# Kernel optimization log

Measured on AMD Instinct MI355X. Metric: run time of the kernel, lower is better.

Reference implementation:

```python
import jax, jax.numpy as jnp
import numpy as np

# Standard FP4 E2M1 lookup table (nvfp4-style): sign bit in nibble MSB.
FP4_LUT = jnp.array([0.0, 0.5, 1.0, 1.5, 2.0, 3.0, 4.0, 6.0,
                     -0.0, -0.5, -1.0, -1.5, -2.0, -3.0, -4.0, -6.0],
                    dtype=jnp.float32)


def dequant_fp4(packed_i32, scales, group_size):
    """packed_i32: [K/8, N] int32 (8 fp4 nibbles per word, low nibble first);
    scales: [K/group_size, N]. Returns dense fp32 weight [K, N]."""
    w = jax.lax.bitcast_convert_type(packed_i32, jnp.uint32)  # [K/8, N]
    # Unpack nibbles along the reduction axis: nibble i -> row 8*r + i.
    nib = jnp.stack([(w >> jnp.uint32(4 * i)) & jnp.uint32(0xF) for i in range(8)],
                    axis=1)                                    # [K/8, 8, N]
    K = nib.shape[0] * 8
    nib = nib.reshape(K, w.shape[1])                           # [K, N]
    vals = FP4_LUT[nib]                                        # [K, N]
    s = jnp.repeat(scales, group_size, axis=0)                 # [K, N]
    return vals * s


def setup_inputs() -> dict:
    key = jax.random.key(0)
    k1, k2, k3, k4, k5, k6 = jax.random.split(key, 6)
    tokens, H, I, G = 4096, 2048, 5632, 128
    return {
        "hidden": jax.random.normal(k1, (tokens, H), dtype=jnp.float32),
        "moe_output": jax.random.normal(k2, (tokens, H), dtype=jnp.float32),
        "gate_up_weights": jax.random.randint(k3, (H // 8, 2 * I), 0, 2147483647, dtype=jnp.int32),
        "gate_up_scales": jax.random.uniform(k4, (H // G, 2 * I), dtype=jnp.float32, minval=0.01, maxval=0.1),
        "down_weights": jax.random.randint(k5, (I // 8, H), 0, 2147483647, dtype=jnp.int32),
        "down_scales": jax.random.uniform(k6, (I // G, H), dtype=jnp.float32, minval=0.01, maxval=0.1),
        "group_size": G,
    }


def reference(hidden, moe_output, gate_up_weights, gate_up_scales,
              down_weights, down_scales, group_size):
    # Shared-expert SwiGLU FFN with FP4 group-quantized weights, fused residual add.
    W_gu = dequant_fp4(gate_up_weights, gate_up_scales, group_size)  # [H, 2I]
    gu = hidden @ W_gu                                               # [T, 2I]
    I = gu.shape[1] // 2
    gate, up = gu[:, :I], gu[:, I:]
    act = jax.nn.silu(gate) * up                                     # [T, I]
    W_d = dequant_fp4(down_weights, down_scales, group_size)         # [I, H]
    return moe_output + act @ W_d                                    # [T, H]
```

## Files before the change

kernel.cpp:

```cpp
#include <hip/hip_runtime.h>
#include <hip/hip_fp16.h>
#include <stdint.h>

#define TOKENS 4096
#define HDIM   2048
#define IDIM   5632
#define BM 128
#define BN 128
#define BK 64

typedef _Float16 f16x8 __attribute__((ext_vector_type(8)));
typedef float    f32x4 __attribute__((ext_vector_type(4)));

__device__ __forceinline__ uint32_t dec2(uint32_t z, uint32_t s2u) {
    uint32_t sgn = (z << 12) & 0x80008000u;
    uint32_t h   = ((z << 9) & 0x0E000E00u) | sgn;
    __half2 hv = __builtin_bit_cast(__half2, h);
    __half2 sv = __builtin_bit_cast(__half2, s2u);
    __half2 r  = __hmul2(hv, sv);
    return __builtin_bit_cast(uint32_t, r);
}
__device__ __forceinline__ int4 dec8(uint32_t w, uint32_t s2u) {
    int4 d;
    d.x = (int)dec2( w        & 0x000F000Fu, s2u);
    d.y = (int)dec2((w >> 4)  & 0x000F000Fu, s2u);
    d.z = (int)dec2((w >> 8)  & 0x000F000Fu, s2u);
    d.w = (int)dec2((w >> 12) & 0x000F000Fu, s2u);
    return d;
}
__device__ __forceinline__ uint32_t scale_s2u(float sc) {
    uint16_t hs = __builtin_bit_cast(uint16_t, __float2half(sc * 16384.0f));
    return (uint32_t)hs * 0x00010001u;
}
__device__ __forceinline__ uint32_t packh(float lo, float hi) {
    __half2 h2 = __halves2half2(__float2half(lo), __float2half(hi));
    return __builtin_bit_cast(uint32_t, h2);
}
__device__ __forceinline__ void gl_lds16(const void* g, void* l) {
    __builtin_amdgcn_global_load_lds(
        (const __attribute__((address_space(1))) uint32_t*)g,
        (__attribute__((address_space(3))) uint32_t*)l, 16, 0, 0);
}

template<bool PRESWZ>
__global__ __launch_bounds__(256) void convert_hidden(
    const float* __restrict__ src, __half* __restrict__ dst)
{
    int idx = blockIdx.x * 256 + threadIdx.x;
    int m  = idx >> 8;
    int kb = idx & 255;
    const float4* s = (const float4*)src + (size_t)idx * 2;
    float4 a = s[0], b = s[1];
    int4 v;
    v.x = (int)packh(a.x, b.x);
    v.y = (int)packh(a.y, b.y);
    v.z = (int)packh(a.z, b.z);
    v.w = (int)packh(a.w, b.w);
    int slot = PRESWZ ? ((kb & 7) ^ (m & 7)) : (kb & 7);
    *(int4*)(dst + (size_t)m * HDIM + (kb & ~7) * 8 + slot * 8) = v;
}

__global__ __launch_bounds__(256) void dequant_wgu(
    const uint32_t* __restrict__ W, const float* __restrict__ S,
    __half* __restrict__ Bt)
{
    int np = blockIdx.x * 256 + threadIdx.x;
    int within = np & 15;
    int pair = np >> 5;
    int sel  = (np >> 4) & 1;
    int sc = pair * 16 + within + (sel ? IDIM : 0);
    int x = np & 7;
    #pragma unroll
    for (int q = 0; q < 4; ++q) {
        int kt = blockIdx.y * 4 + q;
        uint32_t s2u = scale_s2u(S[(size_t)(kt >> 1) * (2 * IDIM) + sc]);
        #pragma unroll
        for (int g = 0; g < 8; ++g) {
            uint32_t w = W[(size_t)(kt * 8 + g) * (2 * IDIM) + sc];
            int4 d = dec8(w, s2u);
            *(int4*)(Bt + (size_t)np * HDIM + kt * 64 + ((g ^ x) << 3)) = d;
        }
    }
}

#define G1_BM 256
#define G1_BN 128
#define G1_NT 32

__global__ __launch_bounds__(512, 1) void gemm1_3buf(
    const __half* __restrict__ A, const __half* __restrict__ Bt,
    __half* __restrict__ act)
{
    __shared__ __half Al[3][G1_BM * 64];
    __shared__ __half Bl[3][G1_BN * 64];
    const int tid  = threadIdx.x;
    const int lane = tid & 63;
    const int wid  = tid >> 6;
    const int wm   = wid >> 1;
    const int wn   = wid & 1;

    int bid = blockIdx.x;
    int swz = (bid & 7) * (1408 / 8) + (bid >> 3);
    int by = swz / 88, bx = swz % 88;
    const int m0 = by * G1_BM;
    const int n0 = bx * G1_BN;

    const __half* pA0 = A  + (size_t)(m0 +   0 + (tid >> 3)) * HDIM + (tid & 7) * 8;
    const __half* pA1 = A  + (size_t)(m0 +  64 + (tid >> 3)) * HDIM + (tid & 7) * 8;
    const __half* pA2 = A  + (size_t)(m0 + 128 + (tid >> 3)) * HDIM + (tid & 7) * 8;
    const __half* pA3 = A  + (size_t)(m0 + 192 + (tid >> 3)) * HDIM + (tid & 7) * 8;
    const __half* pB0 = Bt + (size_t)(n0 +   0 + (tid >> 3)) * HDIM + (tid & 7) * 8;
    const __half* pB1 = Bt + (size_t)(n0 +  64 + (tid >> 3)) * HDIM + (tid & 7) * 8;

    auto stgA = [&](int buf, int kt) {
        gl_lds16(pA0 + (size_t)kt * 64, &Al[buf][(0    + wid * 64) * 8]);
        gl_lds16(pA1 + (size_t)kt * 64, &Al[buf][(512  + wid * 64) * 8]);
        gl_lds16(pA2 + (size_t)kt * 64, &Al[buf][(1024 + wid * 64) * 8]);
        gl_lds16(pA3 + (size_t)kt * 64, &Al[buf][(1536 + wid * 64) * 8]);
    };
    auto stgB = [&](int buf, int kt) {
        gl_lds16(pB0 + (size_t)kt * 64, &Bl[buf][(0    + wid * 64) * 8]);
        gl_lds16(pB1 + (size_t)kt * 64, &Bl[buf][(512  + wid * 64) * 8]);
    };

    f32x4 acc[4][4];
    #pragma unroll
    for (int i = 0; i < 4; ++i)
        #pragma unroll
        for (int j = 0; j < 4; ++j) acc[i][j] = f32x4{0.f, 0.f, 0.f, 0.f};

    stgA(0, 0); stgB(0, 0);
    stgA(1, 1); stgB(1, 1);
    asm volatile("s_waitcnt vmcnt(6)" ::: "memory");
    asm volatile("s_barrier" ::: "memory");

    for (int kt = 0; kt < G1_NT; ++kt) {
        int cur = kt % 3;
        int nxt = cur + 2; if (nxt >= 3) nxt -= 3;
        const bool st = (kt + 2) < G1_NT;
        const __half* Ac = &Al[cur][0];
        const __half* Bc = &Bl[cur][0];

        f16x8 a[2][2], b[4][2];
        #pragma unroll
        for (int mi = 0; mi < 2; ++mi)
            #pragma unroll
            for (int kk = 0; kk < 2; ++kk) {
                int r  = wm * 64 + mi * 16 + (lane & 15);
                int kb = kk * 4 + (lane >> 4);
                a[mi][kk] = *(const f16x8*)&Ac[r * 64 + ((kb ^ (r & 7)) << 3)];
            }
        #pragma unroll
        for (int ni = 0; ni < 4; ++ni)
            #pragma unroll
            for (int kk = 0; kk < 2; ++kk) {
                int r  = wn * 64 + ni * 16 + (lane & 15);
                int kb = kk * 4 + (lane >> 4);
                b[ni][kk] = *(const f16x8*)&Bc[r * 64 + ((kb ^ (r & 7)) << 3)];
            }
        if (st) stgA(nxt, kt + 2);
        asm volatile("s_barrier" ::: "memory");
        asm volatile("s_waitcnt lgkmcnt(0)" ::: "memory");
        __builtin_amdgcn_sched_barrier(0);
        __builtin_amdgcn_s_setprio(1);
        #pragma unroll
        for (int mi = 0; mi < 2; ++mi)
            #pragma unroll
            for (int ni = 0; ni < 4; ++ni)
                #pragma unroll
                for (int kk = 0; kk < 2; ++kk)
                    acc[mi][ni] = __builtin_amdgcn_mfma_f32_16x16x32_f16(a[mi][kk], b[ni][kk], acc[mi][ni], 0, 0, 0);
        __builtin_amdgcn_s_setprio(0);
        asm volatile("s_barrier" ::: "memory");

        f16x8 a2[2][2];
        #pragma unroll
        for (int mi = 0; mi < 2; ++mi)
            #pragma unroll
            for (int kk = 0; kk < 2; ++kk) {
                int r  = wm * 64 + (mi + 2) * 16 + (lane & 15);
                int kb = kk * 4 + (lane >> 4);
                a2[mi][kk] = *(const f16x8*)&Ac[r * 64 + ((kb ^ (r & 7)) << 3)];
            }
        if (st) stgB(nxt, kt + 2);
        asm volatile("s_barrier" ::: "memory");
        asm volatile("s_waitcnt lgkmcnt(0)" ::: "memory");
        __builtin_amdgcn_sched_barrier(0);
        __builtin_amdgcn_s_setprio(1);
        #pragma unroll
        for (int mi = 0; mi < 2; ++mi)
            #pragma unroll
            for (int ni = 0; ni < 4; ++ni)
                #pragma unroll
                for (int kk = 0; kk < 2; ++kk)
                    acc[mi + 2][ni] = __builtin_amdgcn_mfma_f32_16x16x32_f16(a2[mi][kk], b[ni][kk], acc[mi + 2][ni], 0, 0, 0);
        __builtin_amdgcn_s_setprio(0);
        if (st) asm volatile("s_waitcnt vmcnt(6)" ::: "memory");
        else    asm volatile("s_waitcnt vmcnt(0)" ::: "memory");
        asm volatile("s_barrier" ::: "memory");
    }

    #pragma unroll
    for (int mi = 0; mi < 4; ++mi) {
        #pragma unroll
        for (int q = 0; q < 2; ++q) {
            int ip = ((n0 + wn * 64) >> 5) + q;
            int gcol = ip * 16 + (lane & 15);
            int colstore = (gcol & ~7) | (((gcol & 3) << 1) | ((gcol >> 2) & 1));
            #pragma unroll
            for (int r = 0; r < 4; ++r) {
                int m = m0 + wm * 64 + mi * 16 + (lane >> 4) * 4 + r;
                float gv = acc[mi][2 * q][r];
                float uv = acc[mi][2 * q + 1][r];
                float sig = 1.0f / (1.0f + __expf(-gv));
                act[(size_t)m * IDIM + colstore] = __float2half(gv * sig * uv);
            }
        }
    }
}

__global__ __launch_bounds__(256, 2) void gemm1_silu(
    const __half* __restrict__ A, const uint32_t* __restrict__ W,
    const float* __restrict__ S, __half* __restrict__ act)
{
    __shared__ __half Alds[BM * BK];
    __shared__ __half Blds[2][BN * BK];
    const int tid  = threadIdx.x;
    const int lane = tid & 63;
    const int wid  = tid >> 6;
    const int wm = wid >> 1, wn = wid & 1;
    const int m0 = blockIdx.y * BM;
    const int c0 = blockIdx.x * BN;

    f32x4 accg[4][4], accu[4][4];
    #pragma unroll
    for (int i = 0; i < 4; ++i)
        #pragma unroll
        for (int j = 0; j < 4; ++j) {
            accg[i][j] = f32x4{0.f, 0.f, 0.f, 0.f};
            accu[i][j] = f32x4{0.f, 0.f, 0.f, 0.f};
        }

    const int c = tid & 127;
    const int rbase = (tid >> 7) * 4;

    for (int kt = 0; kt < HDIM / BK; ++kt) {
        const int k0 = kt * BK;
        #pragma unroll
        for (int i = 0; i < 4; ++i) {
            int u = tid + i * 256;
            int row = u >> 3, kb = u & 7;
            int4 v = *(const int4*)(A + (size_t)(m0 + row) * HDIM + k0 + kb * 8);
            *(int4*)((char*)Alds + row * 128 + ((kb ^ (row & 7)) << 4)) = v;
        }
        const int g = k0 >> 7;
        #pragma unroll
        for (int p = 0; p < 2; ++p) {
            const int ncol = (p ? IDIM : 0) + c0 + c;
            uint32_t s2u = scale_s2u(S[(size_t)g * (2 * IDIM) + ncol]);
            #pragma unroll
            for (int i = 0; i < 4; ++i) {
                int rl = rbase + i;
                uint32_t w = W[(size_t)(kt * 8 + rl) * (2 * IDIM) + ncol];
                int4 d = dec8(w, s2u);
                *(int4*)((char*)&Blds[p][0] + c * 128 + ((rl ^ (c & 7)) << 4)) = d;
            }
        }
        __syncthreads();
        #pragma unroll
        for (int ks = 0; ks < 2; ++ks) {
            f16x8 af[4], bg[4], bu[4];
            const int kb = ks * 4 + (lane >> 4);
            #pragma unroll
            for (int mi = 0; mi < 4; ++mi) {
                int m = wm * 64 + mi * 16 + (lane & 15);
                af[mi] = *(const f16x8*)((const char*)Alds + m * 128 + ((kb ^ (m & 7)) << 4));
            }
            #pragma unroll
            for (int ni = 0; ni < 4; ++ni) {
                int n = wn * 64 + ni * 16 + (lane & 15);
                bg[ni] = *(const f16x8*)((const char*)&Blds[0][0] + n * 128 + ((kb ^ (n & 7)) << 4));
                bu[ni] = *(const f16x8*)((const char*)&Blds[1][0] + n * 128 + ((kb ^ (n & 7)) << 4));
            }
            #pragma unroll
            for (int mi = 0; mi < 4; ++mi)
                #pragma unroll
                for (int ni = 0; ni < 4; ++ni) {
                    accg[mi][ni] = __builtin_amdgcn_mfma_f32_16x16x32_f16(af[mi], bg[ni], accg[mi][ni], 0, 0, 0);
                    accu[mi][ni] = __builtin_amdgcn_mfma_f32_16x16x32_f16(af[mi], bu[ni], accu[mi][ni], 0, 0, 0);
                }
        }
        __syncthreads();
    }
    #pragma unroll
    for (int mi = 0; mi < 4; ++mi) {
        #pragma unroll
        for (int ni = 0; ni < 4; ++ni) {
            int nlog = c0 + wn * 64 + ni * 16 + (lane & 15);
            int ncol = (nlog & ~7) | (((nlog & 3) << 1) | ((nlog >> 2) & 1));
            #pragma unroll
            for (int r = 0; r < 4; ++r) {
                int m = m0 + wm * 64 + mi * 16 + (lane >> 4) * 4 + r;
                float gv = accg[mi][ni][r];
                float uv = accu[mi][ni][r];
                float sig = 1.0f / (1.0f + __expf(-gv));
                act[(size_t)m * IDIM + ncol] = __float2half(gv * sig * uv);
            }
        }
    }
}

__global__ __launch_bounds__(256, 2) void gemm2_add(
    const __half* __restrict__ A, const uint32_t* __restrict__ W,
    const float* __restrict__ S, const float* __restrict__ moe,
    float* __restrict__ out)
{
    __shared__ __half Alds[BM * BK];
    __shared__ __half Blds[BN * BK];
    const int tid  = threadIdx.x;
    const int lane = tid & 63;
    const int wid  = tid >> 6;
    const int wm = wid >> 1, wn = wid & 1;
    const int m0 = blockIdx.y * BM;
    const int n0 = blockIdx.x * BN;

    f32x4 acc[4][4];
    #pragma unroll
    for (int i = 0; i < 4; ++i)
        #pragma unroll
        for (int j = 0; j < 4; ++j) acc[i][j] = f32x4{0.f, 0.f, 0.f, 0.f};

    const int c = tid & 127;
    const int rbase = (tid >> 7) * 4;

    for (int kt = 0; kt < IDIM / BK; ++kt) {
        const int k0 = kt * BK;
        #pragma unroll
        for (int i = 0; i < 4; ++i) {
            int u = tid + i * 256;
            int row = u >> 3, kb = u & 7;
            int4 v = *(const int4*)(A + (size_t)(m0 + row) * IDIM + k0 + kb * 8);
            *(int4*)((char*)Alds + row * 128 + ((kb ^ (row & 7)) << 4)) = v;
        }
        {
            const int g = k0 >> 7;
            const int ncol = n0 + c;
            uint32_t s2u = scale_s2u(S[(size_t)g * HDIM + ncol]);
            #pragma unroll
            for (int i = 0; i < 4; ++i) {
                int rl = rbase + i;
                uint32_t w = W[(size_t)(kt * 8 + rl) * HDIM + ncol];
                int4 d = dec8(w, s2u);
                *(int4*)((char*)Blds + c * 128 + ((rl ^ (c & 7)) << 4)) = d;
            }
        }
        __syncthreads();
        #pragma unroll
        for (int ks = 0; ks < 2; ++ks) {
            f16x8 af[4], bf[4];
            const int kb = ks * 4 + (lane >> 4);
            #pragma unroll
            for (int mi = 0; mi < 4; ++mi) {
                int m = wm * 64 + mi * 16 + (lane & 15);
                af[mi] = *(const f16x8*)((const char*)Alds + m * 128 + ((kb ^ (m & 7)) << 4));
            }
            #pragma unroll
            for (int ni = 0; ni < 4; ++ni) {
                int n = wn * 64 + ni * 16 + (lane & 15);
                bf[ni] = *(const f16x8*)((const char*)Blds + n * 128 + ((kb ^ (n & 7)) << 4));
            }
            #pragma unroll
            for (int mi = 0; mi < 4; ++mi)
                #pragma unroll
                for (int ni = 0; ni < 4; ++ni)
                    acc[mi][ni] = __builtin_amdgcn_mfma_f32_16x16x32_f16(af[mi], bf[ni], acc[mi][ni], 0, 0, 0);
        }
        __syncthreads();
    }
    #pragma unroll
    for (int mi = 0; mi < 4; ++mi) {
        #pragma unroll
        for (int ni = 0; ni < 4; ++ni) {
            int n = n0 + wn * 64 + ni * 16 + (lane & 15);
            #pragma unroll
            for (int r = 0; r < 4; ++r) {
                int m = m0 + wm * 64 + mi * 16 + (lane >> 4) * 4 + r;
                out[(size_t)m * HDIM + n] = moe[(size_t)m * HDIM + n] + acc[mi][ni][r];
            }
        }
    }
}

extern "C" void kernel_launch(void* const* d_in, const int* in_sizes, int n_in,
                              void* d_out, int out_size, void* d_ws, size_t ws_size,
                              hipStream_t stream) {
    const float*    hidden = (const float*)d_in[0];
    const float*    moe    = (const float*)d_in[1];
    const uint32_t* wgu    = (const uint32_t*)d_in[2];
    const float*    sgu    = (const float*)d_in[3];
    const uint32_t* wd     = (const uint32_t*)d_in[4];
    const float*    sd     = (const float*)d_in[5];
    float* out = (float*)d_out;

    __half* hidden_f16 = (__half*)d_ws;
    __half* act        = (__half*)((char*)d_ws + (size_t)TOKENS * HDIM * 2);
    size_t need = (size_t)TOKENS * HDIM * 2 + (size_t)TOKENS * IDIM * 2
                + (size_t)HDIM * (2 * IDIM) * 2;

    if (ws_size >= need) {
        __half* wgu16 = (__half*)((char*)d_ws + (size_t)TOKENS * HDIM * 2
                                              + (size_t)TOKENS * IDIM * 2);
        convert_hidden<true><<<dim3(TOKENS * HDIM / 8 / 256), dim3(256), 0, stream>>>(hidden, hidden_f16);
        dequant_wgu<<<dim3(2 * IDIM / 256, 8), dim3(256), 0, stream>>>(wgu, sgu, wgu16);
        gemm1_3buf<<<dim3(1408), dim3(512), 0, stream>>>(hidden_f16, wgu16, act);
    } else {
        convert_hidden<false><<<dim3(TOKENS * HDIM / 8 / 256), dim3(256), 0, stream>>>(hidden, hidden_f16);
        gemm1_silu<<<dim3(IDIM / BN, TOKENS / BM), dim3(256), 0, stream>>>(hidden_f16, wgu, sgu, act);
    }
    gemm2_add<<<dim3(HDIM / BN, TOKENS / BM), dim3(256), 0, stream>>>(act, wd, sd, moe, out);
}
```

Measured before the change: 370.3 us.

## Use 256x256 GEMM1 tiles with k-slab weight layout and 8-phase pipeline

The gate/up GEMM now uses 256x256 output tiles per 512-thread block with double-buffered LDS, in place of 256x128 tiles with triple buffering. The goal is more MFMA work per LDS byte and fewer global loads per output. The dequantized weights are now stored as contiguous per-k-tile slabs ([kt][n][64]), so each B stage reads from a compact region. The main loop is split into four MFMA phases, with A/B fragment loads and staging interleaved between them. The larger tile raises register pressure (128 accumulators) and LDS use, and reduces the number of blocks to 704, which may hurt occupancy and load balance.

Result: no change. 369.2 us (-0.3%).

```diff
diff --git a/kernel.cpp b/kernel.cpp
--- a/kernel.cpp
+++ b/kernel.cpp
@@ -8,6 +8,9 @@
 #define BM 128
 #define BN 128
 #define BK 64
+
+#define G1_NP  11264
+#define G1_KSB (G1_NP * 64)
 
 typedef _Float16 f16x8 __attribute__((ext_vector_type(8)));
 typedef float    f32x4 __attribute__((ext_vector_type(4)));
@@ -65,151 +68,174 @@
     __half* __restrict__ Bt)
 {
     int np = blockIdx.x * 256 + threadIdx.x;
+    int kt = blockIdx.y;
     int within = np & 15;
     int pair = np >> 5;
     int sel  = (np >> 4) & 1;
     int sc = pair * 16 + within + (sel ? IDIM : 0);
     int x = np & 7;
-    #pragma unroll
-    for (int q = 0; q < 4; ++q) {
-        int kt = blockIdx.y * 4 + q;
-        uint32_t s2u = scale_s2u(S[(size_t)(kt >> 1) * (2 * IDIM) + sc]);
-        #pragma unroll
-        for (int g = 0; g < 8; ++g) {
-            uint32_t w = W[(size_t)(kt * 8 + g) * (2 * IDIM) + sc];
-            int4 d = dec8(w, s2u);
-            *(int4*)(Bt + (size_t)np * HDIM + kt * 64 + ((g ^ x) << 3)) = d;
-        }
-    }
-}
-
-#define G1_BM 256
-#define G1_BN 128
-#define G1_NT 32
-
-__global__ __launch_bounds__(512, 1) void gemm1_3buf(
+    uint32_t s2u = scale_s2u(S[(size_t)(kt >> 1) * (2 * IDIM) + sc]);
+    uint32_t w[8];
+    #pragma unroll
+    for (int g = 0; g < 8; ++g)
+        w[g] = W[(size_t)(kt * 8 + g) * (2 * IDIM) + sc];
+    __half* dst = Bt + (size_t)kt * G1_KSB + (size_t)np * 64;
+    #pragma unroll
+    for (int s = 0; s < 8; ++s) {
+        int4 d = dec8(w[s ^ x], s2u);
+        *(int4*)(dst + s * 8) = d;
+    }
+}
+
+__global__ __launch_bounds__(512, 2) void gemm1_8ph(
     const __half* __restrict__ A, const __half* __restrict__ Bt,
     __half* __restrict__ act)
 {
-    __shared__ __half Al[3][G1_BM * 64];
-    __shared__ __half Bl[3][G1_BN * 64];
+    __shared__ __half Al[2][256 * 64];
+    __shared__ __half Bl[2][256 * 64];
     const int tid  = threadIdx.x;
     const int lane = tid & 63;
     const int wid  = tid >> 6;
-    const int wm   = wid >> 1;
-    const int wn   = wid & 1;
+    const int wm   = wid >> 2;
+    const int wn   = wid & 3;
 
     int bid = blockIdx.x;
-    int swz = (bid & 7) * (1408 / 8) + (bid >> 3);
-    int by = swz / 88, bx = swz % 88;
-    const int m0 = by * G1_BM;
-    const int n0 = bx * G1_BN;
-
-    const __half* pA0 = A  + (size_t)(m0 +   0 + (tid >> 3)) * HDIM + (tid & 7) * 8;
-    const __half* pA1 = A  + (size_t)(m0 +  64 + (tid >> 3)) * HDIM + (tid & 7) * 8;
-    const __half* pA2 = A  + (size_t)(m0 + 128 + (tid >> 3)) * HDIM + (tid & 7) * 8;
-    const __half* pA3 = A  + (size_t)(m0 + 192 + (tid >> 3)) * HDIM + (tid & 7) * 8;
-    const __half* pB0 = Bt + (size_t)(n0 +   0 + (tid >> 3)) * HDIM + (tid & 7) * 8;
-    const __half* pB1 = Bt + (size_t)(n0 +  64 + (tid >> 3)) * HDIM + (tid & 7) * 8;
-
-    auto stgA = [&](int buf, int kt) {
-        gl_lds16(pA0 + (size_t)kt * 64, &Al[buf][(0    + wid * 64) * 8]);
-        gl_lds16(pA1 + (size_t)kt * 64, &Al[buf][(512  + wid * 64) * 8]);
-        gl_lds16(pA2 + (size_t)kt * 64, &Al[buf][(1024 + wid * 64) * 8]);
-        gl_lds16(pA3 + (size_t)kt * 64, &Al[buf][(1536 + wid * 64) * 8]);
+    int swz = (bid & 7) * 88 + (bid >> 3);
+    int by = swz / 44, bx = swz % 44;
+    const int m0 = by * 256;
+    const int n0 = bx * 256;
+
+    const __half* pAsrc = A  + (size_t)(m0 + (tid >> 3)) * HDIM + (tid & 7) * 8;
+    const __half* pBsrc = Bt + (size_t)(n0 + (tid >> 3)) * 64 + (tid & 7) * 8;
+
+    auto stageA = [&](int buf, int kt) {
+        const __half* s = pAsrc + kt * 64;
+        gl_lds16(s,                      &Al[buf][(0   + wid * 8) * 64]);
+        gl_lds16(s + (size_t)64  * HDIM, &Al[buf][(64  + wid * 8) * 64]);
+        gl_lds16(s + (size_t)128 * HDIM, &Al[buf][(128 + wid * 8) * 64]);
+        gl_lds16(s + (size_t)192 * HDIM, &Al[buf][(192 + wid * 8) * 64]);
     };
-    auto stgB = [&](int buf, int kt) {
-        gl_lds16(pB0 + (size_t)kt * 64, &Bl[buf][(0    + wid * 64) * 8]);
-        gl_lds16(pB1 + (size_t)kt * 64, &Bl[buf][(512  + wid * 64) * 8]);
+    auto stageB = [&](int buf, int kt) {
+        const __half* s = pBsrc + (size_t)kt * G1_KSB;
+        gl_lds16(s,            &Bl[buf][(0   + wid * 8) * 64]);
+        gl_lds16(s + 64  * 64, &Bl[buf][(64  + wid * 8) * 64]);
+        gl_lds16(s + 128 * 64, &Bl[buf][(128 + wid * 8) * 64]);
+        gl_lds16(s + 192 * 64, &Bl[buf][(192 + wid * 8) * 64]);
     };
 
-    f32x4 acc[4][4];
-    #pragma unroll
-    for (int i = 0; i < 4; ++i)
+    f32x4 acc[8][4];
+    #pragma unroll
+    for (int i = 0; i < 8; ++i)
         #pragma unroll
         for (int j = 0; j < 4; ++j) acc[i][j] = f32x4{0.f, 0.f, 0.f, 0.f};
 
-    stgA(0, 0); stgB(0, 0);
-    stgA(1, 1); stgB(1, 1);
-    asm volatile("s_waitcnt vmcnt(6)" ::: "memory");
+    const int rA0 = wm * 128 + (lane & 15);
+    const int rB0 = wn * 64  + (lane & 15);
+    const int xa  = rA0 & 7;
+    const int xb  = rB0 & 7;
+    const int kb0 = lane >> 4;
+
+    stageB(0, 0); stageA(0, 0);
+    stageB(1, 1); stageA(1, 1);
+    asm volatile("s_waitcnt vmcnt(8)" ::: "memory");
     asm volatile("s_barrier" ::: "memory");
 
-    for (int kt = 0; kt < G1_NT; ++kt) {
-        int cur = kt % 3;
-        int nxt = cur + 2; if (nxt >= 3) nxt -= 3;
-        const bool st = (kt + 2) < G1_NT;
+    f16x8 a[4][2], b[4][2];
+    for (int kt = 0; kt < 32; ++kt) {
+        const int cur = kt & 1;
         const __half* Ac = &Al[cur][0];
         const __half* Bc = &Bl[cur][0];
-
-        f16x8 a[2][2], b[4][2];
-        #pragma unroll
-        for (int mi = 0; mi < 2; ++mi)
-            #pragma unroll
-            for (int kk = 0; kk < 2; ++kk) {
-                int r  = wm * 64 + mi * 16 + (lane & 15);
-                int kb = kk * 4 + (lane >> 4);
-                a[mi][kk] = *(const f16x8*)&Ac[r * 64 + ((kb ^ (r & 7)) << 3)];
-            }
-        #pragma unroll
-        for (int ni = 0; ni < 4; ++ni)
-            #pragma unroll
-            for (int kk = 0; kk < 2; ++kk) {
-                int r  = wn * 64 + ni * 16 + (lane & 15);
-                int kb = kk * 4 + (lane >> 4);
-                b[ni][kk] = *(const f16x8*)&Bc[r * 64 + ((kb ^ (r & 7)) << 3)];
-            }
-        if (st) stgA(nxt, kt + 2);
+        const bool st = kt < 30;
+
+        #pragma unroll
+        for (int mi = 0; mi < 4; ++mi)
+            #pragma unroll
+            for (int kk = 0; kk < 2; ++kk)
+                a[mi][kk] = *(const f16x8*)&Ac[(rA0 + mi * 16) * 64 + (((kb0 + kk * 4) ^ xa) << 3)];
+        #pragma unroll
+        for (int ni = 0; ni < 2; ++ni)
+            #pragma unroll
+            for (int kk = 0; kk < 2; ++kk)
+                b[ni][kk] = *(const f16x8*)&Bc[(rB0 + ni * 16) * 64 + (((kb0 + kk * 4) ^ xb) << 3)];
+        asm volatile("s_waitcnt lgkmcnt(8)" ::: "memory");
         asm volatile("s_barrier" ::: "memory");
         asm volatile("s_waitcnt lgkmcnt(0)" ::: "memory");
         __builtin_amdgcn_sched_barrier(0);
         __builtin_amdgcn_s_setprio(1);
         #pragma unroll
-        for (int mi = 0; mi < 2; ++mi)
-            #pragma unroll
-            for (int ni = 0; ni < 4; ++ni)
+        for (int mi = 0; mi < 4; ++mi)
+            #pragma unroll
+            for (int ni = 0; ni < 2; ++ni)
                 #pragma unroll
                 for (int kk = 0; kk < 2; ++kk)
                     acc[mi][ni] = __builtin_amdgcn_mfma_f32_16x16x32_f16(a[mi][kk], b[ni][kk], acc[mi][ni], 0, 0, 0);
         __builtin_amdgcn_s_setprio(0);
         asm volatile("s_barrier" ::: "memory");
 
-        f16x8 a2[2][2];
-        #pragma unroll
-        for (int mi = 0; mi < 2; ++mi)
-            #pragma unroll
-            for (int kk = 0; kk < 2; ++kk) {
-                int r  = wm * 64 + (mi + 2) * 16 + (lane & 15);
-                int kb = kk * 4 + (lane >> 4);
-                a2[mi][kk] = *(const f16x8*)&Ac[r * 64 + ((kb ^ (r & 7)) << 3)];
-            }
-        if (st) stgB(nxt, kt + 2);
+        #pragma unroll
+        for (int ni = 2; ni < 4; ++ni)
+            #pragma unroll
+            for (int kk = 0; kk < 2; ++kk)
+                b[ni][kk] = *(const f16x8*)&Bc[(rB0 + ni * 16) * 64 + (((kb0 + kk * 4) ^ xb) << 3)];
         asm volatile("s_barrier" ::: "memory");
         asm volatile("s_waitcnt lgkmcnt(0)" ::: "memory");
         __builtin_amdgcn_sched_barrier(0);
         __builtin_amdgcn_s_setprio(1);
         #pragma unroll
-        for (int mi = 0; mi < 2; ++mi)
-            #pragma unroll
-            for (int ni = 0; ni < 4; ++ni)
+        for (int mi = 0; mi < 4; ++mi)
+            #pragma unroll
+            for (int ni = 2; ni < 4; ++ni)
                 #pragma unroll
                 for (int kk = 0; kk < 2; ++kk)
-                    acc[mi + 2][ni] = __builtin_amdgcn_mfma_f32_16x16x32_f16(a2[mi][kk], b[ni][kk], acc[mi + 2][ni], 0, 0, 0);
+                    acc[mi][ni] = __builtin_amdgcn_mfma_f32_16x16x32_f16(a[mi][kk], b[ni][kk], acc[mi][ni], 0, 0, 0);
         __builtin_amdgcn_s_setprio(0);
-        if (st) asm volatile("s_waitcnt vmcnt(6)" ::: "memory");
+        asm volatile("s_barrier" ::: "memory");
+
+        #pragma unroll
+        for (int mi = 0; mi < 4; ++mi)
+            #pragma unroll
+            for (int kk = 0; kk < 2; ++kk)
+                a[mi][kk] = *(const f16x8*)&Ac[(rA0 + (mi + 4) * 16) * 64 + (((kb0 + kk * 4) ^ xa) << 3)];
+        if (st) stageB(cur, kt + 2);
+        asm volatile("s_barrier" ::: "memory");
+        asm volatile("s_waitcnt lgkmcnt(0)" ::: "memory");
+        __builtin_amdgcn_sched_barrier(0);
+        __builtin_amdgcn_s_setprio(1);
+        #pragma unroll
+        for (int mi = 0; mi < 4; ++mi)
+            #pragma unroll
+            for (int ni = 2; ni < 4; ++ni)
+                #pragma unroll
+                for (int kk = 0; kk < 2; ++kk)
+                    acc[mi + 4][ni] = __builtin_amdgcn_mfma_f32_16x16x32_f16(a[mi][kk], b[ni][kk], acc[mi + 4][ni], 0, 0, 0);
+        __builtin_amdgcn_s_setprio(0);
+        asm volatile("s_barrier" ::: "memory");
+
+        if (st) stageA(cur, kt + 2);
+        asm volatile("s_barrier" ::: "memory");
+        __builtin_amdgcn_s_setprio(1);
+        #pragma unroll
+        for (int mi = 0; mi < 4; ++mi)
+            #pragma unroll
+            for (int ni = 0; ni < 2; ++ni)
+                #pragma unroll
+                for (int kk = 0; kk < 2; ++kk)
+                    acc[mi + 4][ni] = __builtin_amdgcn_mfma_f32_16x16x32_f16(a[mi][kk], b[ni][kk], acc[mi + 4][ni], 0, 0, 0);
+        __builtin_amdgcn_s_setprio(0);
+        if (st) asm volatile("s_waitcnt vmcnt(8)" ::: "memory");
         else    asm volatile("s_waitcnt vmcnt(0)" ::: "memory");
         asm volatile("s_barrier" ::: "memory");
     }
 
     #pragma unroll
-    for (int mi = 0; mi < 4; ++mi) {
+    for (int mi = 0; mi < 8; ++mi) {
         #pragma unroll
         for (int q = 0; q < 2; ++q) {
-            int ip = ((n0 + wn * 64) >> 5) + q;
-            int gcol = ip * 16 + (lane & 15);
-            int colstore = (gcol & ~7) | (((gcol & 3) << 1) | ((gcol >> 2) & 1));
+            int gc = ((n0 + wn * 64 + q * 32) >> 5) * 16 + (lane & 15);
+            int colstore = (gc & ~7) | (((gc & 3) << 1) | ((gc >> 2) & 1));
             #pragma unroll
             for (int r = 0; r < 4; ++r) {
-                int m = m0 + wm * 64 + mi * 16 + (lane >> 4) * 4 + r;
+                int m = m0 + wm * 128 + mi * 16 + (lane >> 4) * 4 + r;
                 float gv = acc[mi][2 * q][r];
                 float uv = acc[mi][2 * q + 1][r];
                 float sig = 1.0f / (1.0f + __expf(-gv));
@@ -411,8 +437,8 @@
         __half* wgu16 = (__half*)((char*)d_ws + (size_t)TOKENS * HDIM * 2
                                               + (size_t)TOKENS * IDIM * 2);
         convert_hidden<true><<<dim3(TOKENS * HDIM / 8 / 256), dim3(256), 0, stream>>>(hidden, hidden_f16);
-        dequant_wgu<<<dim3(2 * IDIM / 256, 8), dim3(256), 0, stream>>>(wgu, sgu, wgu16);
-        gemm1_3buf<<<dim3(1408), dim3(512), 0, stream>>>(hidden_f16, wgu16, act);
+        dequant_wgu<<<dim3(G1_NP / 256, 32), dim3(256), 0, stream>>>(wgu, sgu, wgu16);
+        gemm1_8ph<<<dim3(704), dim3(512), 0, stream>>>(hidden_f16, wgu16, act);
     } else {
         convert_hidden<false><<<dim3(TOKENS * HDIM / 8 / 256), dim3(256), 0, stream>>>(hidden, hidden_f16);
         gemm1_silu<<<dim3(IDIM / BN, TOKENS / BM), dim3(256), 0, stream>>>(hidden_f16, wgu, sgu, act);
```
